# Optimization experiments

Measured on AMD Instinct MI355X. Metric: run time of the kernel, lower is better.

The kernel has to match this reference:

```python
import jax, jax.numpy as jnp
import numpy as np

N, C, H, W = 4, 256, 128, 128
BLOCK = 8
FWB = H // BLOCK  # feature_size_with_block = 16
N_BBOX = 100
M = N_BBOX * N * FWB * FWB  # 102400 rois


def setup_inputs() -> dict:
    key = jax.random.key(0)
    ks = jax.random.split(key, 6)
    s = 1.0 / np.sqrt(C).astype(np.float32)
    return {
        "feature": jax.random.normal(ks[0], (N, C, H, W), jnp.float32),
        "rois_feature": jax.random.normal(ks[1], (M, C, 1, 1), jnp.float32),
        "W_weight": jax.random.normal(ks[2], (C, C), jnp.float32) * s,
        "b_weight": jnp.zeros((C,), jnp.float32),
        "W_fuse": jax.random.normal(ks[3], (C, C), jnp.float32) * s,
        "b_fuse": jnp.zeros((C,), jnp.float32),
        "W_pw": jax.random.normal(ks[4], (BLOCK * BLOCK, C), jnp.float32) * s,
        "b_pw": jnp.zeros((BLOCK * BLOCK,), jnp.float32),
        "feature_size_with_block": FWB,
    }


def reference(feature, rois_feature, W_weight, b_weight, W_fuse, b_fuse, W_pw, b_pw, feature_size_with_block):
    n, c, h, w = feature.shape
    f = feature_size_with_block
    blk = h // f  # block_size
    m = rois_feature.shape[0]
    n_bbox = m // (n * f * f)

    x = rois_feature[:, :, 0, 0]  # [M, C] (1x1 conv on 1x1 spatial == dense layer)
    feat_w = jax.nn.relu(x @ W_weight.T + b_weight)  # [M, C]
    feat_f = jax.nn.relu(x @ W_fuse.T + b_fuse)      # [M, C]
    point_weight = feat_w @ W_pw.T + b_pw            # [M, B*B]

    # [n_bbox, N, F, F, B, B] -> [N, n_bbox, F, F, B, B]
    pw = point_weight.reshape(n_bbox, n, f, f, blk, blk).transpose(1, 0, 2, 3, 4, 5)
    # feature -> blocks: [N, C, F, B, F, B] -> [N, C, F, F, B, B]
    fb = feature.reshape(n, c, f, blk, f, blk).transpose(0, 1, 2, 4, 3, 5)
    # weighted block-sum without materializing the n_bbox-repeated tensor.
    # torch: sum over (B,B) -> [N,nb,C,F,F], then permute(1,0,3,4,2) -> [nb,N,F,F,C]
    out = jnp.einsum('ncpqab,nkpqab->knpqc', fb, pw)  # [nb, N, F, F, C]
    out = out.reshape(m, c)[:, :, None, None]          # [M, C, 1, 1]
    fused = feat_f[:, :, None, None] + out
    return fused, out
```

## Files before the change

kernel.cpp:

```cpp
#include <hip/hip_runtime.h>

#define NN 4
#define CC 256
#define HH 128
#define FWBv 16
#define BLK 8
#define NBBOX 100
#define MM (NBBOX * NN * FWBv * FWBv)

typedef __attribute__((ext_vector_type(8))) short bf16x8;
typedef __attribute__((ext_vector_type(4))) float f32x4;

__device__ __forceinline__ unsigned short f2bf(float x) {
  union { float f; unsigned int u; } v; v.f = x;
  unsigned int r = v.u + 0x7FFFu + ((v.u >> 16) & 1u);
  return (unsigned short)(r >> 16);
}

__device__ __forceinline__ void async16(const void* g, void* l) {
  __builtin_amdgcn_global_load_lds(
      (__attribute__((address_space(1))) void*)(g),
      (__attribute__((address_space(3))) void*)(l), 16, 0, 0);
}

__global__ __launch_bounds__(256) void k_convert(
    const float* __restrict__ Wf, const float* __restrict__ Ww,
    const float* __restrict__ Wpw,
    unsigned short* __restrict__ oWf, unsigned short* __restrict__ oWw,
    unsigned short* __restrict__ oWpw) {
  int i = blockIdx.x * 256 + threadIdx.x;
  oWf[i] = f2bf(Wf[i]);
  oWw[i] = f2bf(Ww[i]);
  if (i < 64 * 256) oWpw[i] = f2bf(Wpw[i]);
}

__global__ __launch_bounds__(256) void k1(
    const float* __restrict__ rois,
    const unsigned short* __restrict__ Wf,
    const unsigned short* __restrict__ Ww,
    const unsigned short* __restrict__ Wpw,
    const float* __restrict__ bf_, const float* __restrict__ bw_,
    const float* __restrict__ bpw_,
    float* __restrict__ fused_slot,
    float* __restrict__ out_slot)
{
  __shared__ unsigned short xs[64][264];
  __shared__ unsigned short bs[256 * 64];
  const int t = threadIdx.x;
  const int lane = t & 63, w = t >> 6;
  const int lr = lane & 15, quad = lane >> 4;
  const int row_base = blockIdx.x * 64;

#pragma unroll
  for (int i = 0; i < 16; ++i) {
    const int elem = (i * 256 + t) * 4;
    const int r = elem >> 8, c = elem & 255;
    const float4 v = *(const float4*)(rois + (size_t)row_base * 256 + elem);
    unsigned int lo = f2bf(v.x) | ((unsigned int)f2bf(v.y) << 16);
    unsigned int hi = f2bf(v.z) | ((unsigned int)f2bf(v.w) << 16);
    *(uint2*)&xs[r][c] = make_uint2(lo, hi);
  }

  for (int pass = 0; pass < 2; ++pass) {
    const unsigned short* Wp = pass ? Ww : Wf;
    f32x4 acc[4][4];
#pragma unroll
    for (int mt = 0; mt < 4; ++mt)
#pragma unroll
      for (int nt = 0; nt < 4; ++nt) acc[mt][nt] = (f32x4){0.f, 0.f, 0.f, 0.f};

    for (int kc = 0; kc < 4; ++kc) {
      __syncthreads();
#pragma unroll
      for (int i = 0; i < 8; ++i) {
        const int r0 = i * 32 + w * 8;
        const unsigned short* g =
            Wp + (size_t)(r0 + (lane >> 3)) * 256 + kc * 64 + (lane & 7) * 8;
        async16(g, &bs[r0 * 64]);
      }
      __syncthreads();
#pragma unroll
      for (int kt = 0; kt < 2; ++kt) {
        const int kk = kt * 32 + quad * 8;
        bf16x8 a[4], b[4];
#pragma unroll
        for (int mt = 0; mt < 4; ++mt)
          a[mt] = *(const bf16x8*)&xs[mt * 16 + lr][kc * 64 + kk];
#pragma unroll
        for (int nt = 0; nt < 4; ++nt)
          b[nt] = *(const bf16x8*)&bs[(w * 64 + nt * 16 + lr) * 64 + kk];
#pragma unroll
        for (int mt = 0; mt < 4; ++mt)
#pragma unroll
          for (int nt = 0; nt < 4; ++nt)
            acc[mt][nt] = __builtin_amdgcn_mfma_f32_16x16x32_bf16(
                a[mt], b[nt], acc[mt][nt], 0, 0, 0);
      }
    }

    if (pass == 0) {
#pragma unroll
      for (int nt = 0; nt < 4; ++nt) {
        const int gcol = w * 64 + nt * 16 + lr;
        const float bias = bf_[gcol];
#pragma unroll
        for (int mt = 0; mt < 4; ++mt)
#pragma unroll
          for (int r = 0; r < 4; ++r) {
            float vv = acc[mt][nt][r] + bias;
            vv = vv > 0.f ? vv : 0.f;
            fused_slot[(size_t)(row_base + mt * 16 + quad * 4 + r) * 256 + gcol] = vv;
          }
      }
    } else {
      __syncthreads();
#pragma unroll
      for (int nt = 0; nt < 4; ++nt) {
        const int gcol = w * 64 + nt * 16 + lr;
        const float bias = bw_[gcol];
#pragma unroll
        for (int mt = 0; mt < 4; ++mt)
#pragma unroll
          for (int r = 0; r < 4; ++r) {
            float vv = acc[mt][nt][r] + bias;
            vv = vv > 0.f ? vv : 0.f;
            xs[mt * 16 + quad * 4 + r][gcol] = f2bf(vv);
          }
      }
    }
  }

  {
#pragma unroll
    for (int i = 0; i < 8; ++i) {
      const int off = (i * 4 + w) * 512;
      async16((const void*)(Wpw + off + lane * 8), &bs[off]);
    }
    __syncthreads();

    f32x4 acc2[4];
#pragma unroll
    for (int mt = 0; mt < 4; ++mt) acc2[mt] = (f32x4){0.f, 0.f, 0.f, 0.f};
#pragma unroll
    for (int kt = 0; kt < 8; ++kt) {
      const int kk = kt * 32 + quad * 8;
      const bf16x8 b = *(const bf16x8*)&bs[(w * 16 + lr) * 256 + kk];
#pragma unroll
      for (int mt = 0; mt < 4; ++mt) {
        const bf16x8 a = *(const bf16x8*)&xs[mt * 16 + lr][kk];
        acc2[mt] = __builtin_amdgcn_mfma_f32_16x16x32_bf16(a, b, acc2[mt], 0, 0, 0);
      }
    }
    const int j = w * 16 + lr;
    const float bias = bpw_[j];
#pragma unroll
    for (int mt = 0; mt < 4; ++mt)
#pragma unroll
      for (int r = 0; r < 4; ++r)
        out_slot[(size_t)(row_base + mt * 16 + quad * 4 + r) * 256 + j] =
            acc2[mt][r] + bias;
  }
}

__global__ __launch_bounds__(512) void k2(
    const float* __restrict__ feature,
    float* __restrict__ fused_slot,
    float* __restrict__ out_slot)
{
  __shared__ unsigned short fbuf[256][72];
  __shared__ unsigned short pwb[112][72];
  const int t = threadIdx.x;
  const int lane = t & 63, w = t >> 6;
  const int lr = lane & 15, quad = lane >> 4;
  const int bid = blockIdx.x;
  const int n = bid >> 8, p = (bid >> 4) & 15, q = bid & 15;

  if (t < 432) {
    const int r = 100 + t / 36, cw = t % 36;
    *(unsigned int*)&pwb[r][cw * 2] = 0u;
  }

  for (int pi = t; pi < 2048; pi += 512) {
    const int c = pi >> 3, a = pi & 7;
    const float* fp =
        feature + (((size_t)n * 256 + c) * 128 + p * 8 + a) * 128 + q * 8;
    const float4 v0 = *(const float4*)fp;
    const float4 v1 = *(const float4*)(fp + 4);
    unsigned int u0 = f2bf(v0.x) | ((unsigned int)f2bf(v0.y) << 16);
    unsigned int u1 = f2bf(v0.z) | ((unsigned int)f2bf(v0.w) << 16);
    unsigned int u2 = f2bf(v1.x) | ((unsigned int)f2bf(v1.y) << 16);
    unsigned int u3 = f2bf(v1.z) | ((unsigned int)f2bf(v1.w) << 16);
    *(uint4*)&fbuf[c][a * 8] = make_uint4(u0, u1, u2, u3);
  }

  for (int pi = t; pi < 1600; pi += 512) {
    const int k = pi >> 4, ch = pi & 15;
    const float4 v =
        *(const float4*)(out_slot + (size_t)(bid + k * 1024) * 256 + ch * 4);
    unsigned int lo = f2bf(v.x) | ((unsigned int)f2bf(v.y) << 16);
    unsigned int hi = f2bf(v.z) | ((unsigned int)f2bf(v.w) << 16);
    *(uint2*)&pwb[k][ch * 4] = make_uint2(lo, hi);
  }
  __syncthreads();

  f32x4 acc[7][2];
#pragma unroll
  for (int mt = 0; mt < 7; ++mt)
#pragma unroll
    for (int nt = 0; nt < 2; ++nt) acc[mt][nt] = (f32x4){0.f, 0.f, 0.f, 0.f};
#pragma unroll
  for (int kt = 0; kt < 2; ++kt) {
    const int kk = kt * 32 + quad * 8;
    bf16x8 a[7], b[2];
#pragma unroll
    for (int mt = 0; mt < 7; ++mt)
      a[mt] = *(const bf16x8*)&pwb[mt * 16 + lr][kk];
#pragma unroll
    for (int nt = 0; nt < 2; ++nt)
      b[nt] = *(const bf16x8*)&fbuf[w * 32 + nt * 16 + lr][kk];
#pragma unroll
    for (int mt = 0; mt < 7; ++mt)
#pragma unroll
      for (int nt = 0; nt < 2; ++nt)
        acc[mt][nt] =
            __builtin_amdgcn_mfma_f32_16x16x32_bf16(a[mt], b[nt], acc[mt][nt], 0, 0, 0);
  }

#pragma unroll
  for (int mt = 0; mt < 7; ++mt) {
#pragma unroll
    for (int r = 0; r < 4; ++r) {
      const int k = mt * 16 + quad * 4 + r;
      if (k < 100) {
        const size_t rowoff = (size_t)(bid + k * 1024) * 256;
#pragma unroll
        for (int nt = 0; nt < 2; ++nt) {
          const int c = w * 32 + nt * 16 + lr;
          const float val = acc[mt][nt][r];
          out_slot[rowoff + c] = val;
          fused_slot[rowoff + c] = fused_slot[rowoff + c] + val;
        }
      }
    }
  }
}

extern "C" void kernel_launch(void* const* d_in, const int* in_sizes, int n_in,
                              void* d_out, int out_size, void* d_ws, size_t ws_size,
                              hipStream_t stream) {
  const float* feature = (const float*)d_in[0];
  const float* rois = (const float*)d_in[1];
  const float* Ww = (const float*)d_in[2];
  const float* bw = (const float*)d_in[3];
  const float* Wf = (const float*)d_in[4];
  const float* bfv = (const float*)d_in[5];
  const float* Wpw = (const float*)d_in[6];
  const float* bpw = (const float*)d_in[7];

  unsigned short* wsWf = (unsigned short*)d_ws;
  unsigned short* wsWw = wsWf + 256 * 256;
  unsigned short* wsWpw = wsWw + 256 * 256;

  float* fused_slot = (float*)d_out;
  float* out_slot = fused_slot + (size_t)MM * 256;

  k_convert<<<256, 256, 0, stream>>>(Wf, Ww, Wpw, wsWf, wsWw, wsWpw);
  k1<<<MM / 64, 256, 0, stream>>>(rois, wsWf, wsWw, wsWpw, bfv, bw, bpw,
                                  fused_slot, out_slot);
  k2<<<NN * FWBv * FWBv, 512, 0, stream>>>(feature, fused_slot, out_slot);
}
```

Before: 508.2 us.

## Double-buffer weight staging in k1 with swizzled LDS and vectorized epilogue stores

Rewrites the k1 GEMM loop to double-buffer the weight tiles in LDS. The next K-chunk is prefetched with async global-to-LDS loads, and vmcnt waits replace full __syncthreads, so loads overlap the MFMAs. The weight tiles use an XOR-swizzled layout to avoid LDS bank conflicts. The MFMA operands are swapped so that each lane holds 4 consecutive columns, which allows float4 bias loads and float4 global stores for fused_slot and out_slot. The loop relies on hand-written waitcnt and barrier ordering, and it drops the per-chunk barriers, so there is a risk of cross-wave races on the shared buffers.

```diff
diff --git a/kernel.cpp b/kernel.cpp
--- a/kernel.cpp
+++ b/kernel.cpp
@@ -32,6 +32,50 @@
   oWf[i] = f2bf(Wf[i]);
   oWw[i] = f2bf(Ww[i]);
   if (i < 64 * 256) oWpw[i] = f2bf(Wpw[i]);
+}
+
+
+__device__ __forceinline__ void stage_w(const unsigned short* __restrict__ Wp,
+                                        int kc, unsigned short* buf, int w,
+                                        int lane) {
+  const int srcs = ((lane & 3) ^ ((lane >> 3) & 3)) * 8;
+  const int rr = lane >> 2;
+#pragma unroll
+  for (int i = 0; i < 4; ++i) {
+    const int r0 = w * 64 + i * 16;
+    async16(Wp + (size_t)(r0 + rr) * 256 + kc * 32 + srcs, buf + r0 * 32);
+  }
+}
+
+__device__ __forceinline__ void stage_wpw(const unsigned short* __restrict__ Wpw,
+                                          unsigned short* buf, int kc4, int w,
+                                          int lane) {
+  const int srcs = ((lane & 7) ^ ((lane >> 3) & 7)) * 8;
+  const int rr = lane >> 3;
+#pragma unroll
+  for (int i = 0; i < 2; ++i) {
+    const int r0 = w * 16 + i * 8;
+    async16(Wpw + (size_t)(r0 + rr) * 256 + kc4 * 64 + srcs, buf + r0 * 64);
+  }
+}
+
+__device__ __forceinline__ void body16(const unsigned short* buf,
+                                       const unsigned short (*xsp)[264],
+                                       int kcol, int w, int lr, int quad,
+                                       int wslot, f32x4 acc[4][4]) {
+  bf16x8 aw[4], bx[4];
+#pragma unroll
+  for (int nt = 0; nt < 4; ++nt)
+    aw[nt] = *(const bf16x8*)&buf[(w * 64 + nt * 16 + lr) * 32 + wslot];
+#pragma unroll
+  for (int mt = 0; mt < 4; ++mt)
+    bx[mt] = *(const bf16x8*)&xsp[mt * 16 + lr][kcol];
+#pragma unroll
+  for (int mt = 0; mt < 4; ++mt)
+#pragma unroll
+    for (int nt = 0; nt < 4; ++nt)
+      acc[mt][nt] = __builtin_amdgcn_mfma_f32_16x16x32_bf16(
+          aw[nt], bx[mt], acc[mt][nt], 0, 0, 0);
 }
 
 __global__ __launch_bounds__(256) void k1(
@@ -44,12 +88,16 @@
     float* __restrict__ fused_slot,
     float* __restrict__ out_slot)
 {
-  __shared__ unsigned short xs[64][264];
-  __shared__ unsigned short bs[256 * 64];
+  __shared__ __align__(16) unsigned short xs[64][264];
+  __shared__ __align__(16) unsigned short bs[2][8192];
+  unsigned short* bsf = &bs[0][0];
   const int t = threadIdx.x;
   const int lane = t & 63, w = t >> 6;
   const int lr = lane & 15, quad = lane >> 4;
   const int row_base = blockIdx.x * 64;
+  const int wslot = (quad ^ ((lr >> 1) & 3)) << 3;
+
+  stage_w(Wf, 0, &bs[0][0], w, lane);
 
 #pragma unroll
   for (int i = 0; i < 16; ++i) {
@@ -60,105 +108,104 @@
     unsigned int hi = f2bf(v.z) | ((unsigned int)f2bf(v.w) << 16);
     *(uint2*)&xs[r][c] = make_uint2(lo, hi);
   }
-
-  for (int pass = 0; pass < 2; ++pass) {
-    const unsigned short* Wp = pass ? Ww : Wf;
-    f32x4 acc[4][4];
-#pragma unroll
-    for (int mt = 0; mt < 4; ++mt)
-#pragma unroll
-      for (int nt = 0; nt < 4; ++nt) acc[mt][nt] = (f32x4){0.f, 0.f, 0.f, 0.f};
-
-    for (int kc = 0; kc < 4; ++kc) {
-      __syncthreads();
-#pragma unroll
-      for (int i = 0; i < 8; ++i) {
-        const int r0 = i * 32 + w * 8;
-        const unsigned short* g =
-            Wp + (size_t)(r0 + (lane >> 3)) * 256 + kc * 64 + (lane & 7) * 8;
-        async16(g, &bs[r0 * 64]);
+  asm volatile("s_waitcnt vmcnt(0) lgkmcnt(0)" ::: "memory");
+  __builtin_amdgcn_s_barrier();
+
+  f32x4 acc[4][4];
+#pragma unroll
+  for (int mt = 0; mt < 4; ++mt)
+#pragma unroll
+    for (int nt = 0; nt < 4; ++nt) acc[mt][nt] = (f32x4){0.f, 0.f, 0.f, 0.f};
+
+#pragma unroll
+  for (int kc = 0; kc < 8; ++kc) {
+    if (kc < 7) stage_w(Wf, kc + 1, &bs[(kc + 1) & 1][0], w, lane);
+    else        stage_w(Ww, 0, &bs[0][0], w, lane);
+    asm volatile("s_waitcnt vmcnt(4)" ::: "memory");
+    body16(&bs[kc & 1][0], xs, kc * 32 + quad * 8, w, lr, quad, wslot, acc);
+  }
+
+#pragma unroll
+  for (int nt = 0; nt < 4; ++nt) {
+    const int col0 = w * 64 + nt * 16 + quad * 4;
+    const float4 b4 = *(const float4*)(bf_ + col0);
+#pragma unroll
+    for (int mt = 0; mt < 4; ++mt) {
+      float4 v;
+      v.x = acc[mt][nt][0] + b4.x; v.x = v.x > 0.f ? v.x : 0.f;
+      v.y = acc[mt][nt][1] + b4.y; v.y = v.y > 0.f ? v.y : 0.f;
+      v.z = acc[mt][nt][2] + b4.z; v.z = v.z > 0.f ? v.z : 0.f;
+      v.w = acc[mt][nt][3] + b4.w; v.w = v.w > 0.f ? v.w : 0.f;
+      *(float4*)(fused_slot + (size_t)(row_base + mt * 16 + lr) * 256 + col0) = v;
+      acc[mt][nt] = (f32x4){0.f, 0.f, 0.f, 0.f};
+    }
+  }
+
+#pragma unroll
+  for (int kc = 0; kc < 8; ++kc) {
+    if (kc < 7) {
+      stage_w(Ww, kc + 1, &bs[(kc + 1) & 1][0], w, lane);
+      asm volatile("s_waitcnt vmcnt(4)" ::: "memory");
+    } else {
+      asm volatile("s_waitcnt vmcnt(0)" ::: "memory");
+    }
+    body16(&bs[kc & 1][0], xs, kc * 32 + quad * 8, w, lr, quad, wslot, acc);
+  }
+
+  __builtin_amdgcn_s_barrier();
+
+#pragma unroll
+  for (int c = 0; c < 4; ++c) stage_wpw(Wpw, bsf + c * 4096, c, w, lane);
+
+#pragma unroll
+  for (int nt = 0; nt < 4; ++nt) {
+    const int col0 = w * 64 + nt * 16 + quad * 4;
+    const float4 b4 = *(const float4*)(bw_ + col0);
+#pragma unroll
+    for (int mt = 0; mt < 4; ++mt) {
+      float v0 = acc[mt][nt][0] + b4.x; v0 = v0 > 0.f ? v0 : 0.f;
+      float v1 = acc[mt][nt][1] + b4.y; v1 = v1 > 0.f ? v1 : 0.f;
+      float v2 = acc[mt][nt][2] + b4.z; v2 = v2 > 0.f ? v2 : 0.f;
+      float v3 = acc[mt][nt][3] + b4.w; v3 = v3 > 0.f ? v3 : 0.f;
+      unsigned int lo = f2bf(v0) | ((unsigned int)f2bf(v1) << 16);
+      unsigned int hi = f2bf(v2) | ((unsigned int)f2bf(v3) << 16);
+      *(uint2*)&xs[mt * 16 + lr][col0] = make_uint2(lo, hi);
+    }
+  }
+  asm volatile("s_waitcnt vmcnt(0) lgkmcnt(0)" ::: "memory");
+  __builtin_amdgcn_s_barrier();
+
+  f32x4 acc2[4];
+#pragma unroll
+  for (int mt = 0; mt < 4; ++mt) acc2[mt] = (f32x4){0.f, 0.f, 0.f, 0.f};
+#pragma unroll
+  for (int c = 0; c < 4; ++c) {
+#pragma unroll
+    for (int kt = 0; kt < 2; ++kt) {
+      const int sl = ((kt * 4 + quad) ^ (lr & 7)) << 3;
+      const bf16x8 apw =
+          *(const bf16x8*)&bsf[c * 4096 + (w * 16 + lr) * 64 + sl];
+      const int kcol = c * 64 + kt * 32 + quad * 8;
+#pragma unroll
+      for (int mt = 0; mt < 4; ++mt) {
+        const bf16x8 bx = *(const bf16x8*)&xs[mt * 16 + lr][kcol];
+        acc2[mt] =
+            __builtin_amdgcn_mfma_f32_16x16x32_bf16(apw, bx, acc2[mt], 0, 0, 0);
       }
-      __syncthreads();
-#pragma unroll
-      for (int kt = 0; kt < 2; ++kt) {
-        const int kk = kt * 32 + quad * 8;
-        bf16x8 a[4], b[4];
-#pragma unroll
-        for (int mt = 0; mt < 4; ++mt)
-          a[mt] = *(const bf16x8*)&xs[mt * 16 + lr][kc * 64 + kk];
-#pragma unroll
-        for (int nt = 0; nt < 4; ++nt)
-          b[nt] = *(const bf16x8*)&bs[(w * 64 + nt * 16 + lr) * 64 + kk];
-#pragma unroll
-        for (int mt = 0; mt < 4; ++mt)
-#pragma unroll
-          for (int nt = 0; nt < 4; ++nt)
-            acc[mt][nt] = __builtin_amdgcn_mfma_f32_16x16x32_bf16(
-                a[mt], b[nt], acc[mt][nt], 0, 0, 0);
-      }
-    }
-
-    if (pass == 0) {
-#pragma unroll
-      for (int nt = 0; nt < 4; ++nt) {
-        const int gcol = w * 64 + nt * 16 + lr;
-        const float bias = bf_[gcol];
-#pragma unroll
-        for (int mt = 0; mt < 4; ++mt)
-#pragma unroll
-          for (int r = 0; r < 4; ++r) {
-            float vv = acc[mt][nt][r] + bias;
-            vv = vv > 0.f ? vv : 0.f;
-            fused_slot[(size_t)(row_base + mt * 16 + quad * 4 + r) * 256 + gcol] = vv;
-          }
-      }
-    } else {
-      __syncthreads();
-#pragma unroll
-      for (int nt = 0; nt < 4; ++nt) {
-        const int gcol = w * 64 + nt * 16 + lr;
-        const float bias = bw_[gcol];
-#pragma unroll
-        for (int mt = 0; mt < 4; ++mt)
-#pragma unroll
-          for (int r = 0; r < 4; ++r) {
-            float vv = acc[mt][nt][r] + bias;
-            vv = vv > 0.f ? vv : 0.f;
-            xs[mt * 16 + quad * 4 + r][gcol] = f2bf(vv);
-          }
-      }
-    }
-  }
-
+    }
+  }
   {
-#pragma unroll
-    for (int i = 0; i < 8; ++i) {
-      const int off = (i * 4 + w) * 512;
-      async16((const void*)(Wpw + off + lane * 8), &bs[off]);
-    }
-    __syncthreads();
-
-    f32x4 acc2[4];
-#pragma unroll
-    for (int mt = 0; mt < 4; ++mt) acc2[mt] = (f32x4){0.f, 0.f, 0.f, 0.f};
-#pragma unroll
-    for (int kt = 0; kt < 8; ++kt) {
-      const int kk = kt * 32 + quad * 8;
-      const bf16x8 b = *(const bf16x8*)&bs[(w * 16 + lr) * 256 + kk];
-#pragma unroll
-      for (int mt = 0; mt < 4; ++mt) {
-        const bf16x8 a = *(const bf16x8*)&xs[mt * 16 + lr][kk];
-        acc2[mt] = __builtin_amdgcn_mfma_f32_16x16x32_bf16(a, b, acc2[mt], 0, 0, 0);
-      }
-    }
-    const int j = w * 16 + lr;
-    const float bias = bpw_[j];
-#pragma unroll
-    for (int mt = 0; mt < 4; ++mt)
-#pragma unroll
-      for (int r = 0; r < 4; ++r)
-        out_slot[(size_t)(row_base + mt * 16 + quad * 4 + r) * 256 + j] =
-            acc2[mt][r] + bias;
+    const int j0 = w * 16 + quad * 4;
+    const float4 bj = *(const float4*)(bpw_ + j0);
+#pragma unroll
+    for (int mt = 0; mt < 4; ++mt) {
+      float4 v;
+      v.x = acc2[mt][0] + bj.x;
+      v.y = acc2[mt][1] + bj.y;
+      v.z = acc2[mt][2] + bj.z;
+      v.w = acc2[mt][3] + bj.w;
+      *(float4*)(out_slot + (size_t)(row_base + mt * 16 + lr) * 256 + j0) = v;
+    }
   }
 }
 
```

Measured after the change: 466.5 us. 1.09x faster.
